# Kernel optimization log

Measured on AMD Instinct MI355X. Metric: run time of the kernel, lower is better.

The kernel has to match this reference:

```python
import jax, jax.numpy as jnp
import numpy as np

B, T, D = 4, 2048, 1024


def setup_inputs() -> dict:
    key = jax.random.key(0)
    ks = jax.random.split(key, 14)
    s = 0.02
    return {
        "x": jax.random.normal(ks[0], (B, T, D), dtype=jnp.float32),
        "time_decay": jax.random.normal(ks[1], (D,), dtype=jnp.float32) * 0.1,
        "tm_k": jax.random.uniform(ks[2], (D,), dtype=jnp.float32),
        "tm_v": jax.random.uniform(ks[3], (D,), dtype=jnp.float32),
        "tm_r": jax.random.uniform(ks[4], (D,), dtype=jnp.float32),
        "Wk": jax.random.normal(ks[5], (D, D), dtype=jnp.float32) * s,
        "Wv": jax.random.normal(ks[6], (D, D), dtype=jnp.float32) * s,
        "Wr": jax.random.normal(ks[7], (D, D), dtype=jnp.float32) * s,
        "Wo": jax.random.normal(ks[8], (D, D), dtype=jnp.float32) * s,
        "cm_k": jax.random.uniform(ks[9], (D,), dtype=jnp.float32),
        "cm_r": jax.random.uniform(ks[10], (D,), dtype=jnp.float32),
        "Wck": jax.random.normal(ks[11], (D, 4 * D), dtype=jnp.float32) * s,
        "Wcv": jax.random.normal(ks[12], (4 * D, D), dtype=jnp.float32) * s,
        "Wcr": jax.random.normal(ks[13], (D, D), dtype=jnp.float32) * s,
    }


def _shift(x):
    # token shift: prepend zero state (initial last_x), drop last token
    return jnp.concatenate([jnp.zeros_like(x[:, :1]), x[:, :-1]], axis=1)


def reference(x, time_decay, tm_k, tm_v, tm_r, Wk, Wv, Wr, Wo,
              cm_k, cm_r, Wck, Wcv, Wcr):
    # ---- time mixing (WKV recurrence) ----
    shifted = _shift(x)
    xk = x * tm_k + shifted * (1.0 - tm_k)
    xv = x * tm_v + shifted * (1.0 - tm_v)
    xr = x * tm_r + shifted * (1.0 - tm_r)
    k = xk @ Wk            # (B,T,D)
    v = xv @ Wv
    r = jax.nn.sigmoid(xr @ Wr)
    ew = jnp.exp(-jnp.exp(time_decay))  # exp(w), w = -exp(time_decay)

    def step(carry, kv):
        num, den = carry
        kt, vt = kv
        ek = jnp.exp(kt)
        num = ew * num + ek * vt
        den = ew * den + ek
        return (num, den), num / (den + 1e-6)

    init = (jnp.zeros((B, D), x.dtype), jnp.zeros((B, D), x.dtype))
    _, wkv_t = jax.lax.scan(step, init, (jnp.swapaxes(k, 0, 1), jnp.swapaxes(v, 0, 1)))
    wkv = jnp.swapaxes(wkv_t, 0, 1)  # (B,T,D)
    x = x + (r * wkv) @ Wo

    # ---- channel mixing (gated FFN, squared ReLU) ----
    shifted2 = _shift(x)
    xk2 = x * cm_k + shifted2 * (1.0 - cm_k)
    xr2 = x * cm_r + shifted2 * (1.0 - cm_r)
    kh = jnp.square(jax.nn.relu(xk2 @ Wck))  # (B,T,4D)
    v2 = kh @ Wcv
    r2 = jax.nn.sigmoid(xr2 @ Wcr)
    return x + r2 * v2
```

## Files before the change

### kernel.cpp

```cpp
#include <hip/hip_runtime.h>
#include <hip/hip_bf16.h>
#include <math.h>

#define BATCH 4
#define TLEN  2048
#define DIM   1024
#define NROWS (BATCH*TLEN)
#define HDIM  (4*DIM)

typedef __hip_bfloat16 bf16;
typedef __attribute__((ext_vector_type(8))) short   shortx8;
typedef __attribute__((ext_vector_type(4))) float   floatx4;

__device__ __forceinline__ unsigned short f2bf(float f) {
    bf16 h = __float2bfloat16(f);
    return __builtin_bit_cast(unsigned short, h);
}

__device__ __forceinline__ void async16(const void* g, void* l) {
    __builtin_amdgcn_global_load_lds((const __attribute__((address_space(1))) void*)g,
                                     (__attribute__((address_space(3))) void*)l, 16, 0, 0);
}

enum { EP_NONE=0, EP_SIGMOID=1, EP_ADD=2, EP_SQRELU=3, EP_FINAL=4 };

template<int BMT, int MODE, typename OutT>
__global__ __launch_bounds__(256)
void mfma_gemm(const bf16* __restrict__ A, const bf16* __restrict__ Bt,
               OutT* __restrict__ C,
               const float* __restrict__ addv, const bf16* __restrict__ mulv,
               int M, int N, int K)
{
    constexpr int MI    = BMT / 32;
    constexpr int AINST = BMT / 32;
    __shared__ bf16 As[BMT*64];
    __shared__ bf16 Bs[128*64];
    const int tid  = threadIdx.x;
    const int lane = tid & 63;
    const int wave = tid >> 6;
    const int wm   = (wave >> 1) * (BMT/2);
    const int wn   = (wave & 1) * 64;
    const size_t m0 = (size_t)blockIdx.y * BMT;
    const size_t n0 = (size_t)blockIdx.x * 128;

    const int r0 = tid >> 3;
    const int kg = (tid & 7) ^ (r0 & 7);
    const int c0 = kg * 8;
    const bf16* ag[AINST];
    const bf16* bg[4];
    #pragma unroll
    for (int j = 0; j < AINST; ++j) ag[j] = A  + (m0 + r0 + j*32) * K + c0;
    #pragma unroll
    for (int j = 0; j < 4; ++j)     bg[j] = Bt + (n0 + r0 + j*32) * K + c0;

    floatx4 acc[MI][4] = {};

    const int mrow = lane & 15;
    const int kqg  = lane >> 4;
    const int kx   = mrow & 7;

    for (int k0 = 0; k0 < K; k0 += 64) {
        #pragma unroll
        for (int j = 0; j < AINST; ++j) async16(ag[j] + k0, As + (tid + j*256) * 8);
        #pragma unroll
        for (int j = 0; j < 4; ++j)     async16(bg[j] + k0, Bs + (tid + j*256) * 8);
        __syncthreads();

        #pragma unroll
        for (int ks = 0; ks < 2; ++ks) {
            const int kcol = ((ks*4 + kqg) ^ kx) << 3;
            shortx8 af[MI], bfr[4];
            #pragma unroll
            for (int i = 0; i < MI; ++i)
                af[i]  = *(const shortx8*)(As + (wm + i*16 + mrow)*64 + kcol);
            #pragma unroll
            for (int i = 0; i < 4; ++i)
                bfr[i] = *(const shortx8*)(Bs + (wn + i*16 + mrow)*64 + kcol);
            #pragma unroll
            for (int mi = 0; mi < MI; ++mi)
                #pragma unroll
                for (int ni = 0; ni < 4; ++ni)
                    acc[mi][ni] = __builtin_amdgcn_mfma_f32_16x16x32_bf16(
                                      af[mi], bfr[ni], acc[mi][ni], 0, 0, 0);
        }
        __syncthreads();
    }

    const int crow = (lane >> 4) * 4;
    const int ccol = lane & 15;
    #pragma unroll
    for (int mi = 0; mi < MI; ++mi) {
        #pragma unroll
        for (int ni = 0; ni < 4; ++ni) {
            #pragma unroll
            for (int r = 0; r < 4; ++r) {
                size_t row = m0 + wm + mi*16 + crow + r;
                size_t col = n0 + wn + ni*16 + ccol;
                size_t off = row * N + col;
                float v = acc[mi][ni][r];
                if (MODE == EP_SIGMOID)      v = 1.0f / (1.0f + __expf(-v));
                else if (MODE == EP_ADD)     v = addv[off] + v;
                else if (MODE == EP_SQRELU)  { float t = fmaxf(v, 0.0f); v = t * t; }
                else if (MODE == EP_FINAL)   v = addv[off] + __bfloat162float(mulv[off]) * v;
                if (sizeof(OutT) == 2) *(unsigned short*)(C + off) = f2bf(v);
                else                   *(float*)(C + off) = v;
            }
        }
    }
}

__global__ __launch_bounds__(256)
void transpose_bf16_kernel(const float* __restrict__ in, bf16* __restrict__ out,
                           int K, int N)
{
    __shared__ float tile[32][33];
    const int kt = blockIdx.y * 32, nt = blockIdx.x * 32;
    #pragma unroll
    for (int i = threadIdx.y; i < 32; i += 8)
        tile[i][threadIdx.x] = in[(size_t)(kt + i) * N + nt + threadIdx.x];
    __syncthreads();
    #pragma unroll
    for (int i = threadIdx.y; i < 32; i += 8)
        out[(size_t)(nt + i) * K + kt + threadIdx.x] =
            __float2bfloat16(tile[threadIdx.x][i]);
}

__global__ __launch_bounds__(256)
void mix3_kernel(const float4* __restrict__ x,
                 const float4* __restrict__ mk, const float4* __restrict__ mv,
                 const float4* __restrict__ mr,
                 ushort4* __restrict__ ok, ushort4* __restrict__ ov,
                 ushort4* __restrict__ orr)
{
    const int D4 = DIM / 4;
    int e   = blockIdx.x * 256 + threadIdx.x;
    int d4  = e & (D4 - 1);
    int t   = (e >> 8) & (TLEN - 1);
    float4 xc = x[e];
    float4 sh = make_float4(0.f, 0.f, 0.f, 0.f);
    if (t > 0) sh = x[e - D4];
    float4 a = mk[d4], b = mv[d4], c = mr[d4];
    ushort4 u;
    u.x=f2bf(xc.x*a.x+sh.x*(1.f-a.x)); u.y=f2bf(xc.y*a.y+sh.y*(1.f-a.y));
    u.z=f2bf(xc.z*a.z+sh.z*(1.f-a.z)); u.w=f2bf(xc.w*a.w+sh.w*(1.f-a.w));
    ok[e]=u;
    u.x=f2bf(xc.x*b.x+sh.x*(1.f-b.x)); u.y=f2bf(xc.y*b.y+sh.y*(1.f-b.y));
    u.z=f2bf(xc.z*b.z+sh.z*(1.f-b.z)); u.w=f2bf(xc.w*b.w+sh.w*(1.f-b.w));
    ov[e]=u;
    u.x=f2bf(xc.x*c.x+sh.x*(1.f-c.x)); u.y=f2bf(xc.y*c.y+sh.y*(1.f-c.y));
    u.z=f2bf(xc.z*c.z+sh.z*(1.f-c.z)); u.w=f2bf(xc.w*c.w+sh.w*(1.f-c.w));
    orr[e]=u;
}

__global__ __launch_bounds__(256)
void mix2_kernel(const float4* __restrict__ x,
                 const float4* __restrict__ mk, const float4* __restrict__ mr,
                 ushort4* __restrict__ ok, ushort4* __restrict__ orr)
{
    const int D4 = DIM / 4;
    int e   = blockIdx.x * 256 + threadIdx.x;
    int d4  = e & (D4 - 1);
    int t   = (e >> 8) & (TLEN - 1);
    float4 xc = x[e];
    float4 sh = make_float4(0.f, 0.f, 0.f, 0.f);
    if (t > 0) sh = x[e - D4];
    float4 a = mk[d4], c = mr[d4];
    ushort4 u;
    u.x=f2bf(xc.x*a.x+sh.x*(1.f-a.x)); u.y=f2bf(xc.y*a.y+sh.y*(1.f-a.y));
    u.z=f2bf(xc.z*a.z+sh.z*(1.f-a.z)); u.w=f2bf(xc.w*a.w+sh.w*(1.f-a.w));
    ok[e]=u;
    u.x=f2bf(xc.x*c.x+sh.x*(1.f-c.x)); u.y=f2bf(xc.y*c.y+sh.y*(1.f-c.y));
    u.z=f2bf(xc.z*c.z+sh.z*(1.f-c.z)); u.w=f2bf(xc.w*c.w+sh.w*(1.f-c.w));
    orr[e]=u;
}

#define WKV_CHUNK 128
#define WKV_WARM  64
__global__ __launch_bounds__(256)
void wkv_kernel(const bf16* __restrict__ K, const bf16* __restrict__ V,
                const bf16* __restrict__ R, const float* __restrict__ td,
                bf16* __restrict__ out)
{
    int d     = blockIdx.x * 256 + threadIdx.x;
    int chunk = blockIdx.y;
    int b     = blockIdx.z;
    int start = chunk * WKV_CHUNK;
    int t0    = start - WKV_WARM; if (t0 < 0) t0 = 0;

    float ew = __expf(-__expf(td[d]));
    float num = 0.f, den = 0.f;
    size_t base = ((size_t)b * TLEN) * DIM + d;

    for (int t = t0; t < start; ++t) {
        size_t idx = base + (size_t)t * DIM;
        float ek = __expf(__bfloat162float(K[idx]));
        num = ew * num + ek * __bfloat162float(V[idx]);
        den = ew * den + ek;
    }
    for (int t = start; t < start + WKV_CHUNK; ++t) {
        size_t idx = base + (size_t)t * DIM;
        float ek = __expf(__bfloat162float(K[idx]));
        num = ew * num + ek * __bfloat162float(V[idx]);
        den = ew * den + ek;
        out[idx] = __float2bfloat16(__bfloat162float(R[idx]) * (num / (den + 1e-6f)));
    }
}

extern "C" void kernel_launch(void* const* d_in, const int* in_sizes, int n_in,
                              void* d_out, int out_size, void* d_ws, size_t ws_size,
                              hipStream_t stream)
{
    const float* x   = (const float*)d_in[0];
    const float* td  = (const float*)d_in[1];
    const float* tmk = (const float*)d_in[2];
    const float* tmv = (const float*)d_in[3];
    const float* tmr = (const float*)d_in[4];
    const float* Wk  = (const float*)d_in[5];
    const float* Wv  = (const float*)d_in[6];
    const float* Wr  = (const float*)d_in[7];
    const float* Wo  = (const float*)d_in[8];
    const float* cmk = (const float*)d_in[9];
    const float* cmr = (const float*)d_in[10];
    const float* Wck = (const float*)d_in[11];
    const float* Wcv = (const float*)d_in[12];
    const float* Wcr = (const float*)d_in[13];
    float* out = (float*)d_out;

    char* ws = (char*)d_ws;
    const size_t MB = 1024 * 1024;
    bf16*  Wk_t  = (bf16*)(ws +   0*MB);
    bf16*  Wv_t  = (bf16*)(ws +   2*MB);
    bf16*  Wr_t  = (bf16*)(ws +   4*MB);
    bf16*  Wo_t  = (bf16*)(ws +   6*MB);
    bf16*  Wcr_t = (bf16*)(ws +   8*MB);
    bf16*  Wck_t = (bf16*)(ws +  10*MB);
    bf16*  Wcv_t = (bf16*)(ws +  18*MB);
    float* f0    = (float*)(ws + 26*MB);
    bf16*  bA    = (bf16*)(ws +  58*MB);
    bf16*  bB    = (bf16*)(ws +  74*MB);
    bf16*  bC    = (bf16*)(ws +  90*MB);
    bf16*  bD    = (bf16*)(ws + 106*MB);
    bf16*  bE    = (bf16*)(ws + 122*MB);
    bf16*  bF    = (bf16*)(ws + 138*MB);

    const dim3 blk(256);
    const dim3 tblk(32, 8);
    const dim3 mixGrid(NROWS * DIM / 4 / 256);
    const dim3 gemmD(DIM / 128, NROWS / 64);
    const dim3 gemmH(HDIM / 128, NROWS / 128);

    transpose_bf16_kernel<<<dim3(32,32),  tblk, 0, stream>>>(Wk,  Wk_t,  DIM, DIM);
    transpose_bf16_kernel<<<dim3(32,32),  tblk, 0, stream>>>(Wv,  Wv_t,  DIM, DIM);
    transpose_bf16_kernel<<<dim3(32,32),  tblk, 0, stream>>>(Wr,  Wr_t,  DIM, DIM);
    transpose_bf16_kernel<<<dim3(32,32),  tblk, 0, stream>>>(Wo,  Wo_t,  DIM, DIM);
    transpose_bf16_kernel<<<dim3(32,32),  tblk, 0, stream>>>(Wcr, Wcr_t, DIM, DIM);
    transpose_bf16_kernel<<<dim3(128,32), tblk, 0, stream>>>(Wck, Wck_t, DIM, HDIM);
    transpose_bf16_kernel<<<dim3(32,128), tblk, 0, stream>>>(Wcv, Wcv_t, HDIM, DIM);

    mix3_kernel<<<mixGrid, blk, 0, stream>>>((const float4*)x,
        (const float4*)tmk, (const float4*)tmv, (const float4*)tmr,
        (ushort4*)bA, (ushort4*)bB, (ushort4*)bC);

    mfma_gemm<64, EP_NONE, bf16>   <<<gemmD, blk, 0, stream>>>(bA, Wk_t, bD, nullptr, nullptr, NROWS, DIM, DIM);
    mfma_gemm<64, EP_NONE, bf16>   <<<gemmD, blk, 0, stream>>>(bB, Wv_t, bE, nullptr, nullptr, NROWS, DIM, DIM);
    mfma_gemm<64, EP_SIGMOID, bf16><<<gemmD, blk, 0, stream>>>(bC, Wr_t, bF, nullptr, nullptr, NROWS, DIM, DIM);

    dim3 wkvGrid(DIM / 256, TLEN / WKV_CHUNK, BATCH);
    wkv_kernel<<<wkvGrid, blk, 0, stream>>>(bD, bE, bF, td, bF);

    mfma_gemm<64, EP_ADD, float>   <<<gemmD, blk, 0, stream>>>(bF, Wo_t, f0, x, nullptr, NROWS, DIM, DIM);

    mix2_kernel<<<mixGrid, blk, 0, stream>>>((const float4*)f0,
        (const float4*)cmk, (const float4*)cmr, (ushort4*)bE, (ushort4*)bA);

    mfma_gemm<64, EP_SIGMOID, bf16><<<gemmD, blk, 0, stream>>>(bA, Wcr_t, bF, nullptr, nullptr, NROWS, DIM, DIM);

    mfma_gemm<128, EP_SQRELU, bf16><<<gemmH, blk, 0, stream>>>(bE, Wck_t, bA, nullptr, nullptr, NROWS, HDIM, DIM);

    mfma_gemm<64, EP_FINAL, float> <<<gemmD, blk, 0, stream>>>(bA, Wcv_t, out, f0, bF, NROWS, DIM, HDIM);
}
```

Baseline: 594.0 us.

## Batch independent GEMMs and weight transposes into grouped multi-problem launches

Adds a grouped GEMM kernel that dispatches several independent bf16 GEMMs (K/V/R projections, and the channel-mix R and K projections) from a single launch using per-problem descriptors and 128x128 tiles. The seven weight transposes are likewise merged into one launch. The intent is to cut launch overhead and fill the GPU better by running independent GEMMs concurrently, which also uses larger tiles for the square GEMMs. The trade-off is a runtime mode branch in the epilogue and a change in tile shape (64-row to 128-row) for the D-sized GEMMs, which halves the number of blocks per problem.

Result: no change. 589.7 us (-0.7%).

```diff
diff --git a/kernel.cpp b/kernel.cpp
--- a/kernel.cpp
+++ b/kernel.cpp
@@ -109,12 +109,108 @@
     }
 }
 
-__global__ __launch_bounds__(256)
-void transpose_bf16_kernel(const float* __restrict__ in, bf16* __restrict__ out,
-                           int K, int N)
-{
+struct GDesc { const bf16* A; const bf16* Bt; bf16* C; int N; int K; int mode; int ntiles; };
+struct GArgs { GDesc d[3]; };
+
+__global__ __launch_bounds__(256)
+void mfma_gemm_multi(GArgs args, int M)
+{
+    int bx = blockIdx.x, di = 0;
+    while (bx >= args.d[di].ntiles) { bx -= args.d[di].ntiles; ++di; }
+    const bf16* A  = args.d[di].A;
+    const bf16* Bt = args.d[di].Bt;
+    bf16*       C  = args.d[di].C;
+    const int   N  = args.d[di].N;
+    const int   K  = args.d[di].K;
+    const int   mode = args.d[di].mode;
+
+    __shared__ bf16 As[128*64];
+    __shared__ bf16 Bs[128*64];
+    const int tid  = threadIdx.x;
+    const int lane = tid & 63;
+    const int wave = tid >> 6;
+    const int wm   = (wave >> 1) * 64;
+    const int wn   = (wave & 1) * 64;
+    const size_t m0 = (size_t)blockIdx.y * 128;
+    const size_t n0 = (size_t)bx * 128;
+
+    const int r0 = tid >> 3;
+    const int kg = (tid & 7) ^ (r0 & 7);
+    const int c0 = kg * 8;
+    const bf16* ag[4];
+    const bf16* bg[4];
+    #pragma unroll
+    for (int j = 0; j < 4; ++j) {
+        ag[j] = A  + (m0 + r0 + j*32) * K + c0;
+        bg[j] = Bt + (n0 + r0 + j*32) * K + c0;
+    }
+
+    floatx4 acc[4][4] = {};
+
+    const int mrow = lane & 15;
+    const int kqg  = lane >> 4;
+    const int kx   = mrow & 7;
+
+    for (int k0 = 0; k0 < K; k0 += 64) {
+        #pragma unroll
+        for (int j = 0; j < 4; ++j) async16(ag[j] + k0, As + (tid + j*256) * 8);
+        #pragma unroll
+        for (int j = 0; j < 4; ++j) async16(bg[j] + k0, Bs + (tid + j*256) * 8);
+        __syncthreads();
+
+        #pragma unroll
+        for (int ks = 0; ks < 2; ++ks) {
+            const int kcol = ((ks*4 + kqg) ^ kx) << 3;
+            shortx8 af[4], bfr[4];
+            #pragma unroll
+            for (int i = 0; i < 4; ++i) {
+                af[i]  = *(const shortx8*)(As + (wm + i*16 + mrow)*64 + kcol);
+                bfr[i] = *(const shortx8*)(Bs + (wn + i*16 + mrow)*64 + kcol);
+            }
+            #pragma unroll
+            for (int mi = 0; mi < 4; ++mi)
+                #pragma unroll
+                for (int ni = 0; ni < 4; ++ni)
+                    acc[mi][ni] = __builtin_amdgcn_mfma_f32_16x16x32_bf16(
+                                      af[mi], bfr[ni], acc[mi][ni], 0, 0, 0);
+        }
+        __syncthreads();
+    }
+
+    const int crow = (lane >> 4) * 4;
+    const int ccol = lane & 15;
+    #pragma unroll
+    for (int mi = 0; mi < 4; ++mi) {
+        #pragma unroll
+        for (int ni = 0; ni < 4; ++ni) {
+            #pragma unroll
+            for (int r = 0; r < 4; ++r) {
+                size_t row = m0 + wm + mi*16 + crow + r;
+                size_t col = n0 + wn + ni*16 + ccol;
+                float v = acc[mi][ni][r];
+                if (mode == EP_SIGMOID)     v = 1.0f / (1.0f + __expf(-v));
+                else if (mode == EP_SQRELU) { float t = fmaxf(v, 0.0f); v = t * t; }
+                *(unsigned short*)(C + row * N + col) = f2bf(v);
+            }
+        }
+    }
+}
+
+struct TDesc { const float* in; bf16* out; int K; int N; int tiles; int tx; };
+struct TArgs { TDesc d[7]; };
+
+__global__ __launch_bounds__(256)
+void transpose_multi(TArgs args)
+{
+    int t = blockIdx.x, di = 0;
+    while (t >= args.d[di].tiles) { t -= args.d[di].tiles; ++di; }
+    const float* in  = args.d[di].in;
+    bf16*        out = args.d[di].out;
+    const int K = args.d[di].K, N = args.d[di].N, tx = args.d[di].tx;
+    const int bx = t % tx, by = t / tx;
+
     __shared__ float tile[32][33];
-    const int kt = blockIdx.y * 32, nt = blockIdx.x * 32;
+    const int kt = by * 32, nt = bx * 32;
     #pragma unroll
     for (int i = threadIdx.y; i < 32; i += 8)
         tile[i][threadIdx.x] = in[(size_t)(kt + i) * N + nt + threadIdx.x];
@@ -242,40 +338,54 @@
     bf16*  bD    = (bf16*)(ws + 106*MB);
     bf16*  bE    = (bf16*)(ws + 122*MB);
     bf16*  bF    = (bf16*)(ws + 138*MB);
+    bf16*  kh    = bB;
 
     const dim3 blk(256);
-    const dim3 tblk(32, 8);
     const dim3 mixGrid(NROWS * DIM / 4 / 256);
     const dim3 gemmD(DIM / 128, NROWS / 64);
-    const dim3 gemmH(HDIM / 128, NROWS / 128);
-
-    transpose_bf16_kernel<<<dim3(32,32),  tblk, 0, stream>>>(Wk,  Wk_t,  DIM, DIM);
-    transpose_bf16_kernel<<<dim3(32,32),  tblk, 0, stream>>>(Wv,  Wv_t,  DIM, DIM);
-    transpose_bf16_kernel<<<dim3(32,32),  tblk, 0, stream>>>(Wr,  Wr_t,  DIM, DIM);
-    transpose_bf16_kernel<<<dim3(32,32),  tblk, 0, stream>>>(Wo,  Wo_t,  DIM, DIM);
-    transpose_bf16_kernel<<<dim3(32,32),  tblk, 0, stream>>>(Wcr, Wcr_t, DIM, DIM);
-    transpose_bf16_kernel<<<dim3(128,32), tblk, 0, stream>>>(Wck, Wck_t, DIM, HDIM);
-    transpose_bf16_kernel<<<dim3(32,128), tblk, 0, stream>>>(Wcv, Wcv_t, HDIM, DIM);
+
+    {
+        TArgs ta;
+        const float* src[7] = {Wk, Wv, Wr, Wo, Wcr, Wck, Wcv};
+        bf16*       dst[7] = {Wk_t, Wv_t, Wr_t, Wo_t, Wcr_t, Wck_t, Wcv_t};
+        int         kk[7]  = {DIM, DIM, DIM, DIM, DIM, DIM, HDIM};
+        int         nn[7]  = {DIM, DIM, DIM, DIM, DIM, HDIM, DIM};
+        int total = 0;
+        for (int i = 0; i < 7; ++i) {
+            int tx = nn[i] / 32, ty = kk[i] / 32;
+            ta.d[i] = {src[i], dst[i], kk[i], nn[i], tx * ty, tx};
+            total += tx * ty;
+        }
+        transpose_multi<<<dim3(total), dim3(32, 8), 0, stream>>>(ta);
+    }
 
     mix3_kernel<<<mixGrid, blk, 0, stream>>>((const float4*)x,
         (const float4*)tmk, (const float4*)tmv, (const float4*)tmr,
         (ushort4*)bA, (ushort4*)bB, (ushort4*)bC);
 
-    mfma_gemm<64, EP_NONE, bf16>   <<<gemmD, blk, 0, stream>>>(bA, Wk_t, bD, nullptr, nullptr, NROWS, DIM, DIM);
-    mfma_gemm<64, EP_NONE, bf16>   <<<gemmD, blk, 0, stream>>>(bB, Wv_t, bE, nullptr, nullptr, NROWS, DIM, DIM);
-    mfma_gemm<64, EP_SIGMOID, bf16><<<gemmD, blk, 0, stream>>>(bC, Wr_t, bF, nullptr, nullptr, NROWS, DIM, DIM);
+    {
+        GArgs ga;
+        ga.d[0] = {bA, Wk_t, bD, DIM, DIM, EP_NONE,    8};
+        ga.d[1] = {bB, Wv_t, bE, DIM, DIM, EP_NONE,    8};
+        ga.d[2] = {bC, Wr_t, bF, DIM, DIM, EP_SIGMOID, 8};
+        mfma_gemm_multi<<<dim3(24, NROWS/128), blk, 0, stream>>>(ga, NROWS);
+    }
 
     dim3 wkvGrid(DIM / 256, TLEN / WKV_CHUNK, BATCH);
     wkv_kernel<<<wkvGrid, blk, 0, stream>>>(bD, bE, bF, td, bF);
 
-    mfma_gemm<64, EP_ADD, float>   <<<gemmD, blk, 0, stream>>>(bF, Wo_t, f0, x, nullptr, NROWS, DIM, DIM);
+    mfma_gemm<64, EP_ADD, float><<<gemmD, blk, 0, stream>>>(bF, Wo_t, f0, x, nullptr, NROWS, DIM, DIM);
 
     mix2_kernel<<<mixGrid, blk, 0, stream>>>((const float4*)f0,
         (const float4*)cmk, (const float4*)cmr, (ushort4*)bE, (ushort4*)bA);
 
-    mfma_gemm<64, EP_SIGMOID, bf16><<<gemmD, blk, 0, stream>>>(bA, Wcr_t, bF, nullptr, nullptr, NROWS, DIM, DIM);
-
-    mfma_gemm<128, EP_SQRELU, bf16><<<gemmH, blk, 0, stream>>>(bE, Wck_t, bA, nullptr, nullptr, NROWS, HDIM, DIM);
-
-    mfma_gemm<64, EP_FINAL, float> <<<gemmD, blk, 0, stream>>>(bA, Wcv_t, out, f0, bF, NROWS, DIM, HDIM);
-}
+    {
+        GArgs ga;
+        ga.d[0] = {bA, Wcr_t, bF, DIM,  DIM, EP_SIGMOID, 8};
+        ga.d[1] = {bE, Wck_t, kh, HDIM, DIM, EP_SQRELU, 32};
+        ga.d[2] = {nullptr, nullptr, nullptr, 0, 0, 0, 0};
+        mfma_gemm_multi<<<dim3(40, NROWS/128), blk, 0, stream>>>(ga, NROWS);
+    }
+
+    mfma_gemm<64, EP_FINAL, float><<<gemmD, blk, 0, stream>>>(kh, Wcv_t, out, f0, bF, NROWS, DIM, HDIM);
+}
```
